# Kernel optimization log

Measured on AMD Instinct MI355X. Metric: run time of the kernel, lower is better.

Reference implementation:

```python
import jax, jax.numpy as jnp
import numpy as np

NEG_SLOPE = 0.2  # PyG GATConv default leaky_relu slope


def segment_softmax(logits, seg, num_segments):
    # logits: [E, H], seg: [E] destination node ids
    m = jax.ops.segment_max(logits, seg, num_segments=num_segments)
    m = jnp.where(jnp.isfinite(m), m, 0.0)  # empty segments
    e = jnp.exp(logits - m[seg])
    s = jax.ops.segment_sum(e, seg, num_segments=num_segments)
    return e / (s[seg] + 1e-16)


def gat_conv(x, src, dst, W, att_src, att_dst, bias, heads, out_ch, concat, num_nodes):
    # x: [N, F_in], W: [F_in, heads*out_ch], att_*: [heads, out_ch]
    h = (x @ W).reshape(num_nodes, heads, out_ch)            # [N, H, C]
    a_src = jnp.sum(h * att_src, axis=-1)                    # [N, H]
    a_dst = jnp.sum(h * att_dst, axis=-1)                    # [N, H]
    logits = jax.nn.leaky_relu(a_src[src] + a_dst[dst], NEG_SLOPE)  # [E, H]
    alpha = segment_softmax(logits, dst, num_nodes)          # [E, H]
    msg = h[src] * alpha[..., None]                          # [E, H, C]
    out = jax.ops.segment_sum(msg, dst, num_segments=num_nodes)  # [N, H, C]
    out = out.reshape(num_nodes, heads * out_ch) if concat else out.mean(axis=1)
    return out + bias


def setup_inputs() -> dict:
    key = jax.random.key(0)
    ks = jax.random.split(key, 12)
    N, E = 50000, 800000
    F_in, Hd, H, F_out = 256, 128, 2, 64

    def glorot(k, shape):
        fan = shape[0] + shape[-1]
        return jax.random.normal(k, shape, dtype=jnp.float32) * jnp.sqrt(2.0 / fan)

    x = jax.random.normal(ks[0], (N, F_in), dtype=jnp.float32)
    edge_index = jax.random.randint(ks[1], (2, E), 0, N, dtype=jnp.int32)
    return {
        "x": x,
        "edge_index": edge_index,
        "W1": glorot(ks[2], (F_in, H * Hd)),
        "att_src1": glorot(ks[3], (H, Hd)),
        "att_dst1": glorot(ks[4], (H, Hd)),
        "b1": jnp.zeros((H * Hd,), dtype=jnp.float32),
        "W2": glorot(ks[5], (H * Hd, F_out)),
        "att_src2": glorot(ks[6], (1, F_out)),
        "att_dst2": glorot(ks[7], (1, F_out)),
        "b2": jnp.zeros((F_out,), dtype=jnp.float32),
    }


def reference(x, edge_index, W1, att_src1, att_dst1, b1, W2, att_src2, att_dst2, b2):
    N = x.shape[0]
    # PyG GATConv default: add self loops
    ar = jnp.arange(N, dtype=edge_index.dtype)
    src = jnp.concatenate([edge_index[0], ar])
    dst = jnp.concatenate([edge_index[1], ar])
    # dropout layers are identity in eval mode
    h = gat_conv(x, src, dst, W1, att_src1, att_dst1, b1,
                 heads=2, out_ch=128, concat=True, num_nodes=N)
    h = jax.nn.elu(h)
    out = gat_conv(h, src, dst, W2, att_src2, att_dst2, b2,
                   heads=1, out_ch=64, concat=False, num_nodes=N)
    return jax.nn.log_softmax(out, axis=1)
```

## Files before the change

kernel.cpp:

```cpp
#include <hip/hip_runtime.h>

typedef unsigned short u16;
typedef short bf8_t __attribute__((ext_vector_type(8)));
typedef float f32x4 __attribute__((ext_vector_type(4)));

__device__ inline u16 f2bf(float f) {
  unsigned u = __float_as_uint(f);
  u += 0x7FFFu + ((u >> 16) & 1u);
  return (u16)(u >> 16);
}
__device__ inline float bf2f(u16 h) { return __uint_as_float(((unsigned)h) << 16); }
__device__ inline float bflo(unsigned u) { return __uint_as_float(u << 16); }
__device__ inline float bfhi(unsigned u) { return __uint_as_float(u & 0xffff0000u); }

__global__ void tp_kernel(const float* __restrict__ W1, const float* __restrict__ W2,
                          u16* __restrict__ W1T, u16* __restrict__ W2T) {
  int idx = blockIdx.x * 256 + threadIdx.x;
  if (idx < 256 * 256) {
    int m = idx / 256, k = idx % 256;
    W1T[idx] = f2bf(W1[(size_t)k * 256 + m]);
  } else if (idx < 256 * 256 + 64 * 256) {
    int i = idx - 256 * 256;
    int m = i / 256, k = i % 256;
    W2T[i] = f2bf(W2[(size_t)k * 64 + m]);
  }
}

template<int BM, int BN, int BK, int WM, int WN, bool AF32, int EPI>
__global__ __launch_bounds__(256) void mfma_gemm(const void* __restrict__ Ap,
                                                 const u16* __restrict__ Bt,
                                                 u16* __restrict__ C,
                                                 const float* __restrict__ att_s,
                                                 const float* __restrict__ att_d,
                                                 float* __restrict__ a_s,
                                                 float* __restrict__ a_d,
                                                 int N, int K) {
  constexpr int PAD = 8;
  __shared__ u16 As[BM][BK + PAD];
  __shared__ u16 Bs[BN][BK + PAD];
  const int tid = threadIdx.x;
  const int row0 = blockIdx.x * BM;
  const int w = tid >> 6, lane = tid & 63;
  const int wr = (w / (BN / WN)) * WM;
  const int wc = (w % (BN / WN)) * WN;
  constexpr int MF = WM / 16, NF = WN / 16;
  constexpr int CPR = BK / 8;
  f32x4 acc[MF][NF] = {};

  for (int k0 = 0; k0 < K; k0 += BK) {
    constexpr int ACH = BM * CPR;
#pragma unroll
    for (int c = 0; c < ACH; c += 256) {
      int cc = c + tid;
      int r = cc / CPR, kc = cc % CPR;
      int row = row0 + r;
      if (AF32) {
        const float* A = (const float*)Ap;
        float4 v0 = make_float4(0.f, 0.f, 0.f, 0.f), v1 = v0;
        if (row < N) {
          const float* p = A + (size_t)row * K + k0 + kc * 8;
          v0 = *(const float4*)p;
          v1 = *(const float4*)(p + 4);
        }
        u16 tmp[8] = {f2bf(v0.x), f2bf(v0.y), f2bf(v0.z), f2bf(v0.w),
                      f2bf(v1.x), f2bf(v1.y), f2bf(v1.z), f2bf(v1.w)};
        *(uint4*)&As[r][kc * 8] = *(uint4*)tmp;
      } else {
        const u16* A = (const u16*)Ap;
        uint4 v = make_uint4(0, 0, 0, 0);
        if (row < N) v = *(const uint4*)(A + (size_t)row * K + k0 + kc * 8);
        *(uint4*)&As[r][kc * 8] = v;
      }
    }
    constexpr int BCH = BN * CPR;
#pragma unroll
    for (int c = 0; c < BCH; c += 256) {
      int cc = c + tid;
      int r = cc / CPR, kc = cc % CPR;
      *(uint4*)&Bs[r][kc * 8] = *(const uint4*)(Bt + (size_t)r * K + k0 + kc * 8);
    }
    __syncthreads();
    const int lr = lane & 15, lk = (lane >> 4) * 8;
    bf8_t a[MF], b[NF];
#pragma unroll
    for (int mi = 0; mi < MF; ++mi) a[mi] = *(bf8_t*)&As[wr + mi * 16 + lr][lk];
#pragma unroll
    for (int ni = 0; ni < NF; ++ni) b[ni] = *(bf8_t*)&Bs[wc + ni * 16 + lr][lk];
#pragma unroll
    for (int mi = 0; mi < MF; ++mi)
#pragma unroll
      for (int ni = 0; ni < NF; ++ni)
        acc[mi][ni] = __builtin_amdgcn_mfma_f32_16x16x32_bf16(a[mi], b[ni], acc[mi][ni], 0, 0, 0);
    __syncthreads();
  }
#pragma unroll
  for (int mi = 0; mi < MF; ++mi)
#pragma unroll
    for (int ni = 0; ni < NF; ++ni)
#pragma unroll
      for (int r = 0; r < 4; ++r) {
        int row = row0 + wr + mi * 16 + (lane >> 4) * 4 + r;
        int col = wc + ni * 16 + (lane & 15);
        if (row < N) C[(size_t)row * BN + col] = f2bf(acc[mi][ni][r]);
      }

  if (EPI == 1) {
    __shared__ float sm_s[4][64];
    __shared__ float sm_d[4][64];
    float asl[NF], adl[NF];
#pragma unroll
    for (int ni = 0; ni < NF; ++ni) {
      asl[ni] = att_s[wc + ni * 16 + (lane & 15)];
      adl[ni] = att_d[wc + ni * 16 + (lane & 15)];
    }
#pragma unroll
    for (int mi = 0; mi < MF; ++mi)
#pragma unroll
      for (int r = 0; r < 4; ++r) {
        float ps = 0.f, pd = 0.f;
#pragma unroll
        for (int ni = 0; ni < NF; ++ni) {
          float c = acc[mi][ni][r];
          ps += c * asl[ni];
          pd += c * adl[ni];
        }
#pragma unroll
        for (int o = 1; o < 16; o <<= 1) {
          ps += __shfl_xor(ps, o);
          pd += __shfl_xor(pd, o);
        }
        if ((lane & 15) == 0) {
          int row = mi * 16 + (lane >> 4) * 4 + r;
          sm_s[w][row] = ps;
          sm_d[w][row] = pd;
        }
      }
    __syncthreads();
    if (tid < 128) {
      int row = tid & 63, head = tid >> 6;
      int grow = row0 + row;
      if (grow < N) {
        a_s[grow * 2 + head] = sm_s[head * 2 + 0][row] + sm_s[head * 2 + 1][row];
        a_d[grow * 2 + head] = sm_d[head * 2 + 0][row] + sm_d[head * 2 + 1][row];
      }
    }
  } else if (EPI == 2) {
    float asl[NF], adl[NF];
#pragma unroll
    for (int ni = 0; ni < NF; ++ni) {
      asl[ni] = att_s[ni * 16 + (lane & 15)];
      adl[ni] = att_d[ni * 16 + (lane & 15)];
    }
#pragma unroll
    for (int mi = 0; mi < MF; ++mi)
#pragma unroll
      for (int r = 0; r < 4; ++r) {
        float ps = 0.f, pd = 0.f;
#pragma unroll
        for (int ni = 0; ni < NF; ++ni) {
          float c = acc[mi][ni][r];
          ps += c * asl[ni];
          pd += c * adl[ni];
        }
#pragma unroll
        for (int o = 1; o < 16; o <<= 1) {
          ps += __shfl_xor(ps, o);
          pd += __shfl_xor(pd, o);
        }
        int row = row0 + wr + mi * 16 + (lane >> 4) * 4 + r;
        if ((lane & 15) == 0 && row < N) {
          a_s[row] = ps;
          a_d[row] = pd;
        }
      }
  }
}

__global__ void count_kernel(const int* __restrict__ ei, int E, int N,
                             int* __restrict__ counts) {
  int e = blockIdx.x * blockDim.x + threadIdx.x;
  int Et = E + N;
  if (e >= Et) return;
  int d = (e < E) ? ei[E + e] : (e - E);
  atomicAdd(&counts[d], 1);
}

__global__ void block_scan_kernel(const int* __restrict__ counts, int* __restrict__ offsets,
                                  int* __restrict__ bsums, int N) {
  __shared__ int sm[256];
  int tid = threadIdx.x;
  int gid = blockIdx.x * 256 + tid;
  int v = (gid < N) ? counts[gid] : 0;
  int val = v;
  sm[tid] = val;
  __syncthreads();
  for (int off = 1; off < 256; off <<= 1) {
    int o = (tid >= off) ? sm[tid - off] : 0;
    __syncthreads();
    val += o;
    sm[tid] = val;
    __syncthreads();
  }
  if (gid < N) offsets[gid] = val - v;
  if (tid == 255) bsums[blockIdx.x] = val;
}

__global__ void scan_sums_kernel(int* __restrict__ bsums, int* __restrict__ offsets,
                                 int nb, int N) {
  __shared__ int sm[1024];
  int tid = threadIdx.x;
  int v = (tid < nb) ? bsums[tid] : 0;
  int val = v;
  sm[tid] = val;
  __syncthreads();
  for (int off = 1; off < 1024; off <<= 1) {
    int o = (tid >= off) ? sm[tid - off] : 0;
    __syncthreads();
    val += o;
    sm[tid] = val;
    __syncthreads();
  }
  if (tid < nb) bsums[tid] = val - v;
  if (tid == 1023) offsets[N] = val;
}

__global__ void add_base_kernel(int* __restrict__ offsets, int* __restrict__ cursor,
                                const int* __restrict__ bsums, int N) {
  int gid = blockIdx.x * 256 + threadIdx.x;
  if (gid >= N) return;
  int o = offsets[gid] + bsums[blockIdx.x];
  offsets[gid] = o;
  cursor[gid] = o;
}

__global__ void scatter_kernel(const int* __restrict__ ei, int E, int N,
                               int* __restrict__ cursor, int* __restrict__ csr_src) {
  int e = blockIdx.x * blockDim.x + threadIdx.x;
  int Et = E + N;
  if (e >= Et) return;
  int s, d;
  if (e < E) { s = ei[e]; d = ei[E + e]; }
  else       { s = d = e - E; }
  int pos = atomicAdd(&cursor[d], 1);
  csr_src[pos] = s;
}

__global__ void agg1_kernel(const u16* __restrict__ H1, const int* __restrict__ offsets,
                            const int* __restrict__ csr_src,
                            const float* __restrict__ a_src, const float* __restrict__ a_dst,
                            const float* __restrict__ b1, u16* __restrict__ out, int N) {
  __shared__ int4 meta[4][64];
  int wv = threadIdx.x >> 6;
  int lane = threadIdx.x & 63;
  int node = blockIdx.x * 4 + wv;
  if (node >= N) return;
  int off = offsets[node];
  int deg = offsets[node + 1] - off;
  float ad0 = a_dst[node * 2 + 0];
  float ad1 = a_dst[node * 2 + 1];
  bool hi = lane >= 32;
  const char* H1c = (const char*)H1;
  const unsigned loff = (unsigned)(lane * 8);
  float4 acc = make_float4(0.f, 0.f, 0.f, 0.f);
  float den = 0.f;
  const int4* mw = meta[wv];

  auto proc = [&](int4 m) {
    float w = hi ? __int_as_float(m.z) : __int_as_float(m.y);
    uint2 u = *(const uint2*)(H1c + (((unsigned)m.x << 9) + loff));
    den += w;
    acc.x += w * bflo(u.x);
    acc.y += w * bfhi(u.x);
    acc.z += w * bflo(u.y);
    acc.w += w * bfhi(u.y);
  };

  for (int base = 0; base < deg; base += 64) {
    int i = base + lane;
    if (i < deg) {
      int s = csr_src[off + i];
      float l0 = a_src[s * 2 + 0] + ad0;
      float l1 = a_src[s * 2 + 1] + ad1;
      l0 = l0 > 0.f ? l0 : 0.2f * l0;
      l1 = l1 > 0.f ? l1 : 0.2f * l1;
      meta[wv][lane] = make_int4(s, __float_as_int(__expf(l0)), __float_as_int(__expf(l1)), 0);
    }
    int cnt = min(64, deg - base);
    int j = 0;
    for (; j + 4 <= cnt; j += 4) {
      int4 m0 = mw[j], m1 = mw[j + 1], m2 = mw[j + 2], m3 = mw[j + 3];
      proc(m0); proc(m1); proc(m2); proc(m3);
    }
    for (; j < cnt; ++j) proc(mw[j]);
  }
  float inv = 1.f / (den + 1e-16f);
  float4 bb = *(const float4*)(b1 + lane * 4);
  float o0 = acc.x * inv + bb.x;
  float o1 = acc.y * inv + bb.y;
  float o2 = acc.z * inv + bb.z;
  float o3 = acc.w * inv + bb.w;
  o0 = o0 > 0.f ? o0 : expm1f(o0);
  o1 = o1 > 0.f ? o1 : expm1f(o1);
  o2 = o2 > 0.f ? o2 : expm1f(o2);
  o3 = o3 > 0.f ? o3 : expm1f(o3);
  uint2 ov;
  ov.x = (unsigned)f2bf(o0) | ((unsigned)f2bf(o1) << 16);
  ov.y = (unsigned)f2bf(o2) | ((unsigned)f2bf(o3) << 16);
  *(uint2*)(out + (size_t)node * 256 + lane * 4) = ov;
}

__global__ void agg2_kernel(const u16* __restrict__ H2, const int* __restrict__ offsets,
                            const int* __restrict__ csr_src,
                            const float* __restrict__ a_src, const float* __restrict__ a_dst,
                            const float* __restrict__ b2, float* __restrict__ out, int N) {
  __shared__ int2 meta[4][64];
  int wv = threadIdx.x >> 6;
  int lane = threadIdx.x & 63;
  int node = blockIdx.x * 4 + wv;
  if (node >= N) return;
  int off = offsets[node];
  int deg = offsets[node + 1] - off;
  float ad = a_dst[node];
  const char* H2c = (const char*)H2;
  const unsigned loff = (unsigned)(lane * 2);
  float acc = 0.f, den = 0.f;
  const int2* mw = meta[wv];

  auto proc = [&](int2 m) {
    float w = __int_as_float(m.y);
    u16 hv = *(const u16*)(H2c + (((unsigned)m.x << 7) + loff));
    den += w;
    acc += w * bf2f(hv);
  };

  for (int base = 0; base < deg; base += 64) {
    int i = base + lane;
    if (i < deg) {
      int s = csr_src[off + i];
      float l = a_src[s] + ad;
      l = l > 0.f ? l : 0.2f * l;
      meta[wv][lane] = make_int2(s, __float_as_int(__expf(l)));
    }
    int cnt = min(64, deg - base);
    int j = 0;
    for (; j + 4 <= cnt; j += 4) {
      int2 m0 = mw[j], m1 = mw[j + 1], m2 = mw[j + 2], m3 = mw[j + 3];
      proc(m0); proc(m1); proc(m2); proc(m3);
    }
    for (; j < cnt; ++j) proc(mw[j]);
  }
  float v = acc / (den + 1e-16f) + b2[lane];
  float m = v;
  for (int o = 32; o; o >>= 1) m = fmaxf(m, __shfl_xor(m, o));
  float ex = __expf(v - m);
  float sum = ex;
  for (int o = 32; o; o >>= 1) sum += __shfl_xor(sum, o);
  out[(size_t)node * 64 + lane] = v - m - logf(sum);
}

extern "C" void kernel_launch(void* const* d_in, const int* in_sizes, int n_in,
                              void* d_out, int out_size, void* d_ws, size_t ws_size,
                              hipStream_t stream) {
  const float* x   = (const float*)d_in[0];
  const int*   ei  = (const int*)d_in[1];
  const float* W1  = (const float*)d_in[2];
  const float* as1 = (const float*)d_in[3];
  const float* ad1 = (const float*)d_in[4];
  const float* b1  = (const float*)d_in[5];
  const float* W2  = (const float*)d_in[6];
  const float* as2 = (const float*)d_in[7];
  const float* ad2 = (const float*)d_in[8];
  const float* b2  = (const float*)d_in[9];
  float* out = (float*)d_out;

  const int N  = in_sizes[0] / 256;
  const int E  = in_sizes[1] / 2;
  const int Et = E + N;
  const int nb = (N + 255) / 256;

  char* p = (char*)d_ws;
  auto alloc = [&](size_t bytes) -> char* {
    char* r = p;
    p += (bytes + 255) & ~(size_t)255;
    return r;
  };
  u16* H1b     = (u16*)alloc((size_t)N * 256 * 2);
  u16* h1act   = (u16*)alloc((size_t)N * 256 * 2);
  u16* H2b     = (u16*)alloc((size_t)N * 64 * 2);
  u16* W1T     = (u16*)alloc((size_t)256 * 256 * 2);
  u16* W2T     = (u16*)alloc((size_t)64 * 256 * 2);
  float* a_src1 = (float*)alloc((size_t)N * 2 * 4);
  float* a_dst1 = (float*)alloc((size_t)N * 2 * 4);
  float* a_src2 = (float*)alloc((size_t)N * 4);
  float* a_dst2 = (float*)alloc((size_t)N * 4);
  int* counts   = (int*)alloc((size_t)N * 4);
  int* offsets  = (int*)alloc((size_t)(N + 1) * 4);
  int* cursor   = (int*)alloc((size_t)N * 4);
  int* bsums    = (int*)alloc((size_t)1024 * 4);
  int* csr_src  = (int*)alloc((size_t)Et * 4);

  const int tb = 256;

  hipMemsetAsync(counts, 0, (size_t)N * 4, stream);
  count_kernel<<<(Et + tb - 1) / tb, tb, 0, stream>>>(ei, E, N, counts);
  block_scan_kernel<<<nb, 256, 0, stream>>>(counts, offsets, bsums, N);
  scan_sums_kernel<<<1, 1024, 0, stream>>>(bsums, offsets, nb, N);
  add_base_kernel<<<nb, 256, 0, stream>>>(offsets, cursor, bsums, N);
  scatter_kernel<<<(Et + tb - 1) / tb, tb, 0, stream>>>(ei, E, N, cursor, csr_src);

  tp_kernel<<<(256 * 256 + 64 * 256 + tb - 1) / tb, tb, 0, stream>>>(W1, W2, W1T, W2T);

  mfma_gemm<64, 256, 32, 64, 64, true, 1><<<(N + 63) / 64, 256, 0, stream>>>(
      x, W1T, H1b, as1, ad1, a_src1, a_dst1, N, 256);
  agg1_kernel<<<(N + 3) / 4, 256, 0, stream>>>(H1b, offsets, csr_src, a_src1, a_dst1, b1,
                                               h1act, N);

  mfma_gemm<128, 64, 32, 32, 64, false, 2><<<(N + 127) / 128, 256, 0, stream>>>(
      h1act, W2T, H2b, as2, ad2, a_src2, a_dst2, N, 256);
  agg2_kernel<<<(N + 3) / 4, 256, 0, stream>>>(H2b, offsets, csr_src, a_src2, a_dst2, b2,
                                               out, N);
}
```

Baseline: 239.5 us.

## Widen gather loads in aggregation kernels and fuse count with weight transpose

The layer-1 and layer-2 aggregation kernels now load 16-byte chunks per lane instead of 8 or 2 bytes. The wave is split into groups that each handle a different edge in parallel, and partial sums are combined with cross-lane shuffles. The edge-count kernel and the weight transpose/convert kernel are merged into one launch to remove a launch. The aim is fewer, wider memory transactions for the random neighbor gathers, at the cost of extra shuffle reductions and idle lanes on the stores.

```diff
diff --git a/kernel.cpp b/kernel.cpp
--- a/kernel.cpp
+++ b/kernel.cpp
@@ -13,16 +13,27 @@
 __device__ inline float bflo(unsigned u) { return __uint_as_float(u << 16); }
 __device__ inline float bfhi(unsigned u) { return __uint_as_float(u & 0xffff0000u); }
 
-__global__ void tp_kernel(const float* __restrict__ W1, const float* __restrict__ W2,
-                          u16* __restrict__ W1T, u16* __restrict__ W2T) {
-  int idx = blockIdx.x * 256 + threadIdx.x;
-  if (idx < 256 * 256) {
-    int m = idx / 256, k = idx % 256;
-    W1T[idx] = f2bf(W1[(size_t)k * 256 + m]);
-  } else if (idx < 256 * 256 + 64 * 256) {
-    int i = idx - 256 * 256;
-    int m = i / 256, k = i % 256;
-    W2T[i] = f2bf(W2[(size_t)k * 64 + m]);
+__global__ void prep_kernel(const int* __restrict__ ei, int E, int N,
+                            int* __restrict__ counts,
+                            const float* __restrict__ W1, const float* __restrict__ W2,
+                            u16* __restrict__ W1T, u16* __restrict__ W2T, int nbc) {
+  if ((int)blockIdx.x < nbc) {
+    int e = blockIdx.x * 256 + threadIdx.x;
+    int Et = E + N;
+    if (e < Et) {
+      int d = (e < E) ? ei[E + e] : (e - E);
+      atomicAdd(&counts[d], 1);
+    }
+  } else {
+    int idx = (blockIdx.x - nbc) * 256 + threadIdx.x;
+    if (idx < 256 * 256) {
+      int m = idx / 256, k = idx % 256;
+      W1T[idx] = f2bf(W1[(size_t)k * 256 + m]);
+    } else if (idx < 256 * 256 + 64 * 256) {
+      int i = idx - 256 * 256;
+      int m = i / 256, k = i % 256;
+      W2T[i] = f2bf(W2[(size_t)k * 64 + m]);
+    }
   }
 }
 
@@ -176,15 +187,6 @@
   }
 }
 
-__global__ void count_kernel(const int* __restrict__ ei, int E, int N,
-                             int* __restrict__ counts) {
-  int e = blockIdx.x * blockDim.x + threadIdx.x;
-  int Et = E + N;
-  if (e >= Et) return;
-  int d = (e < E) ? ei[E + e] : (e - E);
-  atomicAdd(&counts[d], 1);
-}
-
 __global__ void block_scan_kernel(const int* __restrict__ counts, int* __restrict__ offsets,
                                   int* __restrict__ bsums, int N) {
   __shared__ int sm[256];
@@ -258,21 +260,24 @@
   int deg = offsets[node + 1] - off;
   float ad0 = a_dst[node * 2 + 0];
   float ad1 = a_dst[node * 2 + 1];
-  bool hi = lane >= 32;
+  const int half = lane >> 5;
+  const int l5 = lane & 31;
+  const bool head1 = (l5 >= 16);
   const char* H1c = (const char*)H1;
-  const unsigned loff = (unsigned)(lane * 8);
-  float4 acc = make_float4(0.f, 0.f, 0.f, 0.f);
+  const unsigned loff = (unsigned)(l5 * 16);
+  float acc[8] = {0.f, 0.f, 0.f, 0.f, 0.f, 0.f, 0.f, 0.f};
   float den = 0.f;
   const int4* mw = meta[wv];
 
-  auto proc = [&](int4 m) {
-    float w = hi ? __int_as_float(m.z) : __int_as_float(m.y);
-    uint2 u = *(const uint2*)(H1c + (((unsigned)m.x << 9) + loff));
+  auto proc = [&](int jj) {
+    int4 m = mw[jj];
+    float w = head1 ? __int_as_float(m.z) : __int_as_float(m.y);
+    uint4 u = *(const uint4*)(H1c + (((unsigned)m.x << 9) + loff));
     den += w;
-    acc.x += w * bflo(u.x);
-    acc.y += w * bfhi(u.x);
-    acc.z += w * bflo(u.y);
-    acc.w += w * bfhi(u.y);
+    acc[0] += w * bflo(u.x); acc[1] += w * bfhi(u.x);
+    acc[2] += w * bflo(u.y); acc[3] += w * bfhi(u.y);
+    acc[4] += w * bflo(u.z); acc[5] += w * bfhi(u.z);
+    acc[6] += w * bflo(u.w); acc[7] += w * bfhi(u.w);
   };
 
   for (int base = 0; base < deg; base += 64) {
@@ -287,26 +292,28 @@
     }
     int cnt = min(64, deg - base);
     int j = 0;
-    for (; j + 4 <= cnt; j += 4) {
-      int4 m0 = mw[j], m1 = mw[j + 1], m2 = mw[j + 2], m3 = mw[j + 3];
-      proc(m0); proc(m1); proc(m2); proc(m3);
-    }
-    for (; j < cnt; ++j) proc(mw[j]);
-  }
+    for (; j + 8 <= cnt; j += 8) {
+      proc(j + half); proc(j + 2 + half); proc(j + 4 + half); proc(j + 6 + half);
+    }
+    for (; j + 2 <= cnt; j += 2) proc(j + half);
+    if (j < cnt && half == 0) proc(j);
+  }
+#pragma unroll
+  for (int k = 0; k < 8; ++k) acc[k] += __shfl_xor(acc[k], 32);
+  den += __shfl_xor(den, 32);
+
   float inv = 1.f / (den + 1e-16f);
-  float4 bb = *(const float4*)(b1 + lane * 4);
-  float o0 = acc.x * inv + bb.x;
-  float o1 = acc.y * inv + bb.y;
-  float o2 = acc.z * inv + bb.z;
-  float o3 = acc.w * inv + bb.w;
-  o0 = o0 > 0.f ? o0 : expm1f(o0);
-  o1 = o1 > 0.f ? o1 : expm1f(o1);
-  o2 = o2 > 0.f ? o2 : expm1f(o2);
-  o3 = o3 > 0.f ? o3 : expm1f(o3);
-  uint2 ov;
-  ov.x = (unsigned)f2bf(o0) | ((unsigned)f2bf(o1) << 16);
-  ov.y = (unsigned)f2bf(o2) | ((unsigned)f2bf(o3) << 16);
-  *(uint2*)(out + (size_t)node * 256 + lane * 4) = ov;
+  float4 b01 = *(const float4*)(b1 + l5 * 8);
+  float4 b23 = *(const float4*)(b1 + l5 * 8 + 4);
+  float bb[8] = {b01.x, b01.y, b01.z, b01.w, b23.x, b23.y, b23.z, b23.w};
+  u16 tmp[8];
+#pragma unroll
+  for (int k = 0; k < 8; ++k) {
+    float o = acc[k] * inv + bb[k];
+    o = o > 0.f ? o : expm1f(o);
+    tmp[k] = f2bf(o);
+  }
+  if (half == 0) *(uint4*)(out + (size_t)node * 256 + l5 * 8) = *(uint4*)tmp;
 }
 
 __global__ void agg2_kernel(const u16* __restrict__ H2, const int* __restrict__ offsets,
@@ -321,16 +328,23 @@
   int off = offsets[node];
   int deg = offsets[node + 1] - off;
   float ad = a_dst[node];
+  const int grp = lane >> 3;
+  const int l3 = lane & 7;
   const char* H2c = (const char*)H2;
-  const unsigned loff = (unsigned)(lane * 2);
-  float acc = 0.f, den = 0.f;
+  const unsigned loff = (unsigned)(l3 * 16);
+  float acc[8] = {0.f, 0.f, 0.f, 0.f, 0.f, 0.f, 0.f, 0.f};
+  float den = 0.f;
   const int2* mw = meta[wv];
 
-  auto proc = [&](int2 m) {
+  auto proc = [&](int jj) {
+    int2 m = mw[jj];
     float w = __int_as_float(m.y);
-    u16 hv = *(const u16*)(H2c + (((unsigned)m.x << 7) + loff));
+    uint4 u = *(const uint4*)(H2c + (((unsigned)m.x << 7) + loff));
     den += w;
-    acc += w * bf2f(hv);
+    acc[0] += w * bflo(u.x); acc[1] += w * bfhi(u.x);
+    acc[2] += w * bflo(u.y); acc[3] += w * bfhi(u.y);
+    acc[4] += w * bflo(u.z); acc[5] += w * bfhi(u.z);
+    acc[6] += w * bflo(u.w); acc[7] += w * bfhi(u.w);
   };
 
   for (int base = 0; base < deg; base += 64) {
@@ -343,19 +357,47 @@
     }
     int cnt = min(64, deg - base);
     int j = 0;
-    for (; j + 4 <= cnt; j += 4) {
-      int2 m0 = mw[j], m1 = mw[j + 1], m2 = mw[j + 2], m3 = mw[j + 3];
-      proc(m0); proc(m1); proc(m2); proc(m3);
-    }
-    for (; j < cnt; ++j) proc(mw[j]);
-  }
-  float v = acc / (den + 1e-16f) + b2[lane];
-  float m = v;
-  for (int o = 32; o; o >>= 1) m = fmaxf(m, __shfl_xor(m, o));
-  float ex = __expf(v - m);
-  float sum = ex;
-  for (int o = 32; o; o >>= 1) sum += __shfl_xor(sum, o);
-  out[(size_t)node * 64 + lane] = v - m - logf(sum);
+    for (; j + 16 <= cnt; j += 16) { proc(j + grp); proc(j + 8 + grp); }
+    for (; j + 8 <= cnt; j += 8) proc(j + grp);
+    int r = cnt - j;
+    if (r > 0 && grp < r) proc(j + grp);
+  }
+#pragma unroll
+  for (int k = 0; k < 8; ++k) {
+    acc[k] += __shfl_xor(acc[k], 8);
+    acc[k] += __shfl_xor(acc[k], 16);
+    acc[k] += __shfl_xor(acc[k], 32);
+  }
+  den += __shfl_xor(den, 8);
+  den += __shfl_xor(den, 16);
+  den += __shfl_xor(den, 32);
+
+  float inv = 1.f / (den + 1e-16f);
+  float4 b01 = *(const float4*)(b2 + l3 * 8);
+  float4 b23 = *(const float4*)(b2 + l3 * 8 + 4);
+  float bb[8] = {b01.x, b01.y, b01.z, b01.w, b23.x, b23.y, b23.z, b23.w};
+  float v[8];
+#pragma unroll
+  for (int k = 0; k < 8; ++k) v[k] = acc[k] * inv + bb[k];
+  float m = v[0];
+#pragma unroll
+  for (int k = 1; k < 8; ++k) m = fmaxf(m, v[k]);
+  m = fmaxf(m, __shfl_xor(m, 1));
+  m = fmaxf(m, __shfl_xor(m, 2));
+  m = fmaxf(m, __shfl_xor(m, 4));
+  float sum = 0.f;
+#pragma unroll
+  for (int k = 0; k < 8; ++k) sum += __expf(v[k] - m);
+  sum += __shfl_xor(sum, 1);
+  sum += __shfl_xor(sum, 2);
+  sum += __shfl_xor(sum, 4);
+  float ls = m + logf(sum);
+  if (lane < 8) {
+    float4 o0 = make_float4(v[0] - ls, v[1] - ls, v[2] - ls, v[3] - ls);
+    float4 o1 = make_float4(v[4] - ls, v[5] - ls, v[6] - ls, v[7] - ls);
+    *(float4*)(out + (size_t)node * 64 + l3 * 8) = o0;
+    *(float4*)(out + (size_t)node * 64 + l3 * 8 + 4) = o1;
+  }
 }
 
 extern "C" void kernel_launch(void* const* d_in, const int* in_sizes, int n_in,
@@ -377,6 +419,8 @@
   const int E  = in_sizes[1] / 2;
   const int Et = E + N;
   const int nb = (N + 255) / 256;
+  const int nbc = (Et + 255) / 256;
+  const int nbt = (256 * 256 + 64 * 256 + 255) / 256;
 
   char* p = (char*)d_ws;
   auto alloc = [&](size_t bytes) -> char* {
@@ -402,14 +446,12 @@
   const int tb = 256;
 
   hipMemsetAsync(counts, 0, (size_t)N * 4, stream);
-  count_kernel<<<(Et + tb - 1) / tb, tb, 0, stream>>>(ei, E, N, counts);
+  prep_kernel<<<nbc + nbt, tb, 0, stream>>>(ei, E, N, counts, W1, W2, W1T, W2T, nbc);
   block_scan_kernel<<<nb, 256, 0, stream>>>(counts, offsets, bsums, N);
   scan_sums_kernel<<<1, 1024, 0, stream>>>(bsums, offsets, nb, N);
   add_base_kernel<<<nb, 256, 0, stream>>>(offsets, cursor, bsums, N);
   scatter_kernel<<<(Et + tb - 1) / tb, tb, 0, stream>>>(ei, E, N, cursor, csr_src);
 
-  tp_kernel<<<(256 * 256 + 64 * 256 + tb - 1) / tb, tb, 0, stream>>>(W1, W2, W1T, W2T);
-
   mfma_gemm<64, 256, 32, 64, 64, true, 1><<<(N + 63) / 64, 256, 0, stream>>>(
       x, W1T, H1b, as1, ad1, a_src1, a_dst1, N, 256);
   agg1_kernel<<<(N + 3) / 4, 256, 0, stream>>>(H1b, offsets, csr_src, a_src1, a_dst1, b1,
```

Result: faster. 233.1 us (-2.7%).
